# Kernel optimization log

Hardware: AMD Instinct MI355X
Metric: run time of the kernel (lower is better)

The kernel has to match this reference:

```python
import jax, jax.numpy as jnp
import numpy as np

K = 8
NMS_RADIUS = 5
SCORE_THRESHOLD = 0.05
SIGMA = 5.0


def setup_inputs() -> dict:
    key = jax.random.key(0)
    k1, k2 = jax.random.split(key)
    heatmap = jax.random.normal(k1, (16, 1, 256, 256), dtype=jnp.float32)
    feature_map = jax.random.normal(k2, (16, 128, 256, 256), dtype=jnp.float32)
    return {"heatmap": heatmap, "feature_map": feature_map}


def _extract_topk_peaks(heatmap):
    # heatmap: [B, 1, H, W]
    B, _, H, W = heatmap.shape
    hm = heatmap[:, 0]  # [B, H, W]
    r = NMS_RADIUS
    # max-pool NMS with -inf padding (== torch pad(-inf) + max_pool2d)
    hm_max = jax.lax.reduce_window(
        hm, -jnp.inf, jax.lax.max,
        window_dimensions=(1, 2 * r + 1, 2 * r + 1),
        window_strides=(1, 1, 1),
        padding=((0, 0), (r, r), (r, r)))
    gmax = jnp.max(hm.reshape(B, -1), axis=1).reshape(B, 1, 1)
    is_peak = (hm >= hm_max) & (hm >= gmax * SCORE_THRESHOLD)
    flat_hm = hm.reshape(B, -1)
    flat_peak = is_peak.reshape(B, -1)
    flat_scores = flat_hm * flat_peak.astype(flat_hm.dtype) \
        + (~flat_peak).astype(flat_hm.dtype) * (-1e9)
    topk_scores, topk_idx = jax.lax.top_k(flat_scores, K)  # [B, K]
    rows = topk_idx // W
    cols = topk_idx % W
    positions = jnp.stack([rows.astype(jnp.float32), cols.astype(jnp.float32)], axis=-1)  # [B,K,2]
    probs = jax.nn.softmax(topk_scores, axis=-1)
    valid = topk_scores > -1e8
    return positions, probs, valid


def _bilinear_sample_at_peaks(feature_map, positions):
    # feature_map: [B, C, H, W], positions: [B, K, 2] (row, col) pixel coords
    # torch grid_sample(align_corners=True, zeros pad): coords stay in-bounds,
    # so clipped bilinear interpolation is exact.
    B, C, H, W = feature_map.shape
    fmt = jnp.transpose(feature_map, (0, 2, 3, 1))  # [B, H, W, C]
    rr = positions[..., 0]
    cc = positions[..., 1]
    r0 = jnp.floor(rr)
    c0 = jnp.floor(cc)
    wr = rr - r0  # [B, K]
    wc = cc - c0
    r0i = jnp.clip(r0.astype(jnp.int32), 0, H - 1)
    r1i = jnp.clip(r0.astype(jnp.int32) + 1, 0, H - 1)
    c0i = jnp.clip(c0.astype(jnp.int32), 0, W - 1)
    c1i = jnp.clip(c0.astype(jnp.int32) + 1, 0, W - 1)
    b = jnp.arange(B)[:, None]  # [B, 1]
    f00 = fmt[b, r0i, c0i]  # [B, K, C]
    f01 = fmt[b, r0i, c1i]
    f10 = fmt[b, r1i, c0i]
    f11 = fmt[b, r1i, c1i]
    wr = wr[..., None]
    wc = wc[..., None]
    return (f00 * (1 - wr) * (1 - wc) + f01 * (1 - wr) * wc
            + f10 * wr * (1 - wc) + f11 * wr * wc)  # [B, K, C]


def _reweight_heatmap(heatmap, positions, weights, valid):
    # heatmap: [B,1,H,W]; positions: [B,K,2]; weights/valid: [B,K]
    B, _, H, W = heatmap.shape
    grid_r = jnp.arange(H, dtype=jnp.float32)[:, None]  # [H, 1]
    grid_c = jnp.arange(W, dtype=jnp.float32)[None, :]  # [1, W]
    pr = positions[:, :, 0][:, :, None, None]  # [B, K, 1, 1]
    pc = positions[:, :, 1][:, :, None, None]
    pw = weights[:, :, None, None]
    pv = valid.astype(jnp.float32)[:, :, None, None]
    dist_sq = (grid_r - pr) ** 2 + (grid_c - pc) ** 2  # [B, K, H, W]
    gaussians = jnp.exp(-dist_sq / (2.0 * SIGMA ** 2)) * pw * pv
    weight_map = jnp.sum(gaussians, axis=1, keepdims=True)  # [B, 1, H, W]
    weight_map = weight_map / (jnp.max(weight_map, axis=(-1, -2), keepdims=True) + 1e-8)
    return heatmap * (0.5 + 0.5 * weight_map)


def reference(heatmap, feature_map):
    positions, probs, valid = _extract_topk_peaks(heatmap)
    peak_feats = _bilinear_sample_at_peaks(feature_map, positions)
    reweighted = _reweight_heatmap(heatmap, positions, probs, valid)
    return reweighted, peak_feats, positions, probs, valid
```

## Files before the change

### kernel.cpp

```cpp
#include <hip/hip_runtime.h>
#include <math.h>

#define NB 16
#define HH 256
#define WW 256
#define NC 128
#define KTOP 8
#define RAD 5
#define TCAP 125
#define TILE_ROWS 16
#define HALO 5
#define LROWS (TILE_ROWS + 2*HALO)


__global__ void k_nms(const float* __restrict__ hm,
                      float* __restrict__ gpart, int* __restrict__ tcount,
                      float* __restrict__ tv, int* __restrict__ ti) {
    int b    = blockIdx.x >> 4;
    int tile = blockIdx.x & 15;
    int row0 = tile * TILE_ROWS;
    int tid  = threadIdx.x;

    __shared__ float t[LROWS][WW];
    __shared__ float hx[LROWS][WW];
    __shared__ int   cnt;
    __shared__ float red[256];
    if (tid == 0) cnt = 0;

    const float4* p4 = (const float4*)(hm + (size_t)b * HH * WW);
    float4 nf = make_float4(-INFINITY, -INFINITY, -INFINITY, -INFINITY);
    for (int i = tid; i < LROWS * (WW / 4); i += 256) {
        int lr = i >> 6, c4 = i & 63;
        int gr = row0 - HALO + lr;
        float4 v = (gr >= 0 && gr < HH) ? p4[gr * 64 + c4] : nf;
        ((float4*)&t[lr][0])[c4] = v;
    }
    __syncthreads();

    for (int i = tid; i < LROWS * WW; i += 256) {
        int lr = i >> 8, col = i & 255;
        int c0 = col - RAD < 0 ? 0 : col - RAD;
        int c1 = col + RAD > WW - 1 ? WW - 1 : col + RAD;
        float m = -INFINITY;
        for (int c = c0; c <= c1; ++c) m = fmaxf(m, t[lr][c]);
        hx[lr][col] = m;
    }
    __syncthreads();

    float tmax = -INFINITY;
    int tile_id = blockIdx.x;
    for (int i = tid; i < TILE_ROWS * WW; i += 256) {
        int lr = (i >> 8) + HALO, col = i & 255;
        float v = t[lr][col];
        tmax = fmaxf(tmax, v);
        float m = -INFINITY;
        for (int r = lr - RAD; r <= lr + RAD; ++r) m = fmaxf(m, hx[r][col]);
        if (v >= m) {
            int pos = atomicAdd(&cnt, 1);
            if (pos < TCAP) {
                tv[tile_id * TCAP + pos] = v;
                ti[tile_id * TCAP + pos] = (row0 + lr - HALO) * WW + col;
            }
        }
    }
    red[tid] = tmax;
    __syncthreads();
    for (int s = 128; s > 0; s >>= 1) {
        if (tid < s) red[tid] = fmaxf(red[tid], red[tid + s]);
        __syncthreads();
    }
    if (tid == 0) {
        gpart[tile_id]  = red[0];
        tcount[tile_id] = cnt > TCAP ? TCAP : cnt;
    }
}

__device__ __forceinline__ float wm_at_f(float fi, float fj,
                                         const float* qr, const float* qc, const float* qw) {
    float wmv = 0.f;
#pragma unroll
    for (int k = 0; k < KTOP; ++k) {
        float dr = fi - qr[k];
        float dc = fj - qc[k];
        wmv += qw[k] * __expf(-(dr * dr + dc * dc) * 0.02f);
    }
    return wmv;
}

__global__ void k_select(const float* __restrict__ fmap,
                         const float* __restrict__ gpart, const int* __restrict__ tcount,
                         const float* __restrict__ tv, const int* __restrict__ ti,
                         float* __restrict__ out_feats, float* __restrict__ out_pos,
                         float* __restrict__ out_probs, float* __restrict__ out_valid,
                         float* __restrict__ pr, float* __restrict__ pc, float* __restrict__ pw,
                         float* __restrict__ winv) {
    int b = blockIdx.x, tid = threadIdx.x;

    __shared__ float cv[16 * TCAP];
    __shared__ int   ci[16 * TCAP];
    __shared__ int   cnt;
    __shared__ int   sct[16];
    __shared__ float red[256];
    __shared__ int   redi[128];
    __shared__ float sel_v[KTOP]; __shared__ int sel_i[KTOP]; __shared__ int sel_p[KTOP];
    __shared__ float s_r[KTOP], s_c[KTOP], s_w[KTOP];

    if (tid == 0) {
        cnt = 0;
        float g = -INFINITY;
        for (int j = 0; j < 16; ++j) g = fmaxf(g, gpart[b * 16 + j]);
        red[0] = 0.05f * g;
    }
    if (tid < 16) sct[tid] = tcount[b * 16 + tid];
    __syncthreads();
    float thresh = red[0];

    for (int i = tid; i < 16 * TCAP; i += 256) {
        int j = i / TCAP, p = i - j * TCAP;
        if (p < sct[j]) {
            float v = tv[(b * 16 + j) * TCAP + p];
            if (v >= thresh) {
                int pos = atomicAdd(&cnt, 1);
                cv[pos] = v;
                ci[pos] = ti[(b * 16 + j) * TCAP + p];
            }
        }
    }
    __syncthreads();
    int count = cnt;

    for (int k = 0; k < KTOP; ++k) {
        float bv = -INFINITY; int bi = 0x7fffffff; int bp = -1;
        for (int i = tid; i < count; i += 256) {
            float v = cv[i]; int idx = ci[i];
            if (v > bv || (v == bv && idx < bi)) { bv = v; bi = idx; bp = i; }
        }
        for (int s = 1; s < 64; s <<= 1) {
            float v = __shfl_xor(bv, s); int idx = __shfl_xor(bi, s); int p = __shfl_xor(bp, s);
            if (v > bv || (v == bv && idx < bi)) { bv = v; bi = idx; bp = p; }
        }
        if ((tid & 63) == 0) { int w = tid >> 6; red[w] = bv; redi[w] = bi; redi[64 + w] = bp; }
        __syncthreads();
        if (tid == 0) {
            float v0 = red[0]; int i0 = redi[0]; int p0 = redi[64];
            for (int j = 1; j < 4; ++j)
                if (red[j] > v0 || (red[j] == v0 && redi[j] < i0)) {
                    v0 = red[j]; i0 = redi[j]; p0 = redi[64 + j];
                }
            sel_v[k] = v0; sel_i[k] = i0; sel_p[k] = p0;
            if (p0 >= 0) cv[p0] = -INFINITY;
        }
        __syncthreads();
    }

    if (tid == 0) {
        int next = 0;
        for (int k = 0; k < KTOP; ++k) {
            if (sel_p[k] < 0) {
                for (;;) {
                    bool taken = false;
                    for (int j = 0; j < count; ++j) if (ci[j] == next) { taken = true; break; }
                    if (!taken) break;
                    ++next;
                }
                sel_i[k] = next;
                sel_v[k] = -1.0e9f;
                ++next;
            }
        }
        float m = sel_v[0];
        for (int k = 1; k < KTOP; ++k) m = fmaxf(m, sel_v[k]);
        float e[KTOP], s = 0.f;
        for (int k = 0; k < KTOP; ++k) { e[k] = expf(sel_v[k] - m); s += e[k]; }
        for (int k = 0; k < KTOP; ++k) {
            float prob = e[k] / s;
            int idx = sel_i[k];
            float rrow = (float)(idx / WW);
            float rcol = (float)(idx % WW);
            float vld  = sel_v[k] > -1.0e8f ? 1.f : 0.f;
            out_pos[(b * KTOP + k) * 2 + 0] = rrow;
            out_pos[(b * KTOP + k) * 2 + 1] = rcol;
            out_probs[b * KTOP + k] = prob;
            out_valid[b * KTOP + k] = vld;
            pr[b * KTOP + k] = rrow;
            pc[b * KTOP + k] = rcol;
            pw[b * KTOP + k] = prob * vld;
            s_r[k] = rrow; s_c[k] = rcol; s_w[k] = prob * vld;
        }
    }
    __syncthreads();

    float m = 0.f;
    for (int i = tid; i < KTOP * 529; i += 256) {
        int k = i / 529, o = i - k * 529;
        int rr = (int)s_r[k] + (o / 23) - 11;
        int cc = (int)s_c[k] + (o % 23) - 11;
        if (rr >= 0 && rr < HH && cc >= 0 && cc < WW)
            m = fmaxf(m, wm_at_f((float)rr, (float)cc, s_r, s_c, s_w));
    }
    red[tid] = m;
    __syncthreads();
    for (int s = 128; s > 0; s >>= 1) {
        if (tid < s) red[tid] = fmaxf(red[tid], red[tid + s]);
        __syncthreads();
    }
    if (tid == 0) winv[b] = 0.5f / (red[0] + 1e-8f);

    for (int t = tid; t < KTOP * NC; t += 256) {
        int k  = t >> 7;
        int ch = t & 127;
        int r = (int)s_r[k];
        int c = (int)s_c[k];
        out_feats[(size_t)b * KTOP * NC + t] = fmap[((size_t)b * NC + ch) * HH * WW + r * WW + c];
    }
}

__global__ void k_reweight(const float* __restrict__ hm,
                           const float* __restrict__ pr, const float* __restrict__ pc,
                           const float* __restrict__ pw, const float* __restrict__ winv,
                           float* __restrict__ out) {
    int tile = blockIdx.x, b = blockIdx.y, tid = threadIdx.x;
    int row0 = tile * TILE_ROWS;

    __shared__ float fc[KTOP][WW];
    __shared__ float ar[KTOP][TILE_ROWS];
    __shared__ float qr[KTOP], qc[KTOP], qw[KTOP];
    __shared__ float qinv;

    if (tid < KTOP) {
        qr[tid] = pr[b * KTOP + tid];
        qc[tid] = pc[b * KTOP + tid];
        qw[tid] = pw[b * KTOP + tid];
    }
    if (tid == 0) qinv = winv[b];
    __syncthreads();

    for (int i = tid; i < KTOP * WW; i += 256) {
        int k = i >> 8, col = i & 255;
        float d = (float)col - qc[k];
        fc[k][col] = __expf(-d * d * 0.02f);
    }
    if (tid < KTOP * TILE_ROWS) {
        int k = tid >> 4, r = tid & 15;
        float d = (float)(row0 + r) - qr[k];
        ar[k][r] = qw[k] * __expf(-d * d * 0.02f);
    }
    __syncthreads();
    float inv = qinv;

    int r  = tid >> 4;
    int cb = (tid & 15) * 4;
    float a[KTOP];
#pragma unroll
    for (int k = 0; k < KTOP; ++k) a[k] = ar[k][r];

    const float4* h4 = (const float4*)(hm + (size_t)b * HH * WW + (size_t)(row0 + r) * WW);
    float4*       o4 = (float4*)(out + (size_t)b * HH * WW + (size_t)(row0 + r) * WW);
#pragma unroll
    for (int u = 0; u < 4; ++u) {
        int c4 = cb + u;
        float4 h = h4[c4];
        float4 w = make_float4(0.f, 0.f, 0.f, 0.f);
#pragma unroll
        for (int k = 0; k < KTOP; ++k) {
            float4 f = ((const float4*)&fc[k][0])[c4];
            w.x += a[k] * f.x;
            w.y += a[k] * f.y;
            w.z += a[k] * f.z;
            w.w += a[k] * f.w;
        }
        float4 o;
        o.x = h.x * (0.5f + w.x * inv);
        o.y = h.y * (0.5f + w.y * inv);
        o.z = h.z * (0.5f + w.z * inv);
        o.w = h.w * (0.5f + w.w * inv);
        o4[c4] = o;
    }
}

extern "C" void kernel_launch(void* const* d_in, const int* in_sizes, int n_in,
                              void* d_out, int out_size, void* d_ws, size_t ws_size,
                              hipStream_t stream) {
    const float* heatmap = (const float*)d_in[0];
    const float* fmap    = (const float*)d_in[1];

    float* out = (float*)d_out;
    float* out_reweighted = out;
    float* out_feats      = out + 1048576;
    float* out_pos        = out + 1048576 + 16384;
    float* out_probs      = out_pos + 256;
    float* out_valid      = out_probs + 128;

    char* ws = (char*)d_ws;
    float* tv     = (float*)(ws + 0);
    int*   ti     = (int*)  (ws + 128000);
    int*   tcount = (int*)  (ws + 256000);
    float* gpart  = (float*)(ws + 257024);
    float* pr     = (float*)(ws + 258048);
    float* pc     = (float*)(ws + 258560);
    float* pw     = (float*)(ws + 259072);
    float* winv   = (float*)(ws + 259584);

    k_nms<<<NB * 16, 256, 0, stream>>>(heatmap, gpart, tcount, tv, ti);
    k_select<<<NB, 256, 0, stream>>>(fmap, gpart, tcount, tv, ti,
                                     out_feats, out_pos, out_probs, out_valid,
                                     pr, pc, pw, winv);
    k_reweight<<<dim3(16, NB), 256, 0, stream>>>(heatmap, pr, pc, pw, winv, out_reweighted);
}
```

Measured before the change: 60.54 us.

## Fuse select and reweight kernels, recomputing top-k selection redundantly per tile

```diff
diff --git a/kernel.cpp b/kernel.cpp
--- a/kernel.cpp
+++ b/kernel.cpp
@@ -7,10 +7,12 @@
 #define NC 128
 #define KTOP 8
 #define RAD 5
-#define TCAP 125
+#define TCAP 128
 #define TILE_ROWS 16
 #define HALO 5
 #define LROWS (TILE_ROWS + 2*HALO)
+#define NT 16
+#define CTOT (NT * TCAP)
 
 
 __global__ void k_nms(const float* __restrict__ hm,
@@ -87,23 +89,26 @@
     return wmv;
 }
 
-__global__ void k_select(const float* __restrict__ fmap,
-                         const float* __restrict__ gpart, const int* __restrict__ tcount,
-                         const float* __restrict__ tv, const int* __restrict__ ti,
-                         float* __restrict__ out_feats, float* __restrict__ out_pos,
-                         float* __restrict__ out_probs, float* __restrict__ out_valid,
-                         float* __restrict__ pr, float* __restrict__ pc, float* __restrict__ pw,
-                         float* __restrict__ winv) {
-    int b = blockIdx.x, tid = threadIdx.x;
-
-    __shared__ float cv[16 * TCAP];
-    __shared__ int   ci[16 * TCAP];
+__global__ void __launch_bounds__(256)
+k_fused(const float* __restrict__ hm, const float* __restrict__ fmap,
+        const float* __restrict__ gpart, const int* __restrict__ tcount,
+        const float* __restrict__ tv, const int* __restrict__ ti,
+        float* __restrict__ out_rw, float* __restrict__ out_feats,
+        float* __restrict__ out_pos, float* __restrict__ out_probs,
+        float* __restrict__ out_valid) {
+    int tile = blockIdx.x, b = blockIdx.y, tid = threadIdx.x;
+    int row0 = tile * TILE_ROWS;
+
+    __shared__ float cv[CTOT];
+    __shared__ int   ci[CTOT];
     __shared__ int   cnt;
     __shared__ int   sct[16];
     __shared__ float red[256];
     __shared__ int   redi[128];
     __shared__ float sel_v[KTOP]; __shared__ int sel_i[KTOP]; __shared__ int sel_p[KTOP];
     __shared__ float s_r[KTOP], s_c[KTOP], s_w[KTOP];
+    __shared__ float fc[KTOP][WW];
+    __shared__ float sq;
 
     if (tid == 0) {
         cnt = 0;
@@ -115,8 +120,8 @@
     __syncthreads();
     float thresh = red[0];
 
-    for (int i = tid; i < 16 * TCAP; i += 256) {
-        int j = i / TCAP, p = i - j * TCAP;
+    for (int i = tid; i < CTOT; i += 256) {
+        int j = i >> 7, p = i & 127;
         if (p < sct[j]) {
             float v = tv[(b * 16 + j) * TCAP + p];
             if (v >= thresh) {
@@ -178,17 +183,22 @@
             float rrow = (float)(idx / WW);
             float rcol = (float)(idx % WW);
             float vld  = sel_v[k] > -1.0e8f ? 1.f : 0.f;
-            out_pos[(b * KTOP + k) * 2 + 0] = rrow;
-            out_pos[(b * KTOP + k) * 2 + 1] = rcol;
-            out_probs[b * KTOP + k] = prob;
-            out_valid[b * KTOP + k] = vld;
-            pr[b * KTOP + k] = rrow;
-            pc[b * KTOP + k] = rcol;
-            pw[b * KTOP + k] = prob * vld;
+            if (tile == 0) {
+                out_pos[(b * KTOP + k) * 2 + 0] = rrow;
+                out_pos[(b * KTOP + k) * 2 + 1] = rcol;
+                out_probs[b * KTOP + k] = prob;
+                out_valid[b * KTOP + k] = vld;
+            }
             s_r[k] = rrow; s_c[k] = rcol; s_w[k] = prob * vld;
         }
     }
     __syncthreads();
+
+    for (int i = tid; i < KTOP * WW; i += 256) {
+        int k = i >> 8, col = i & 255;
+        float d = (float)col - s_c[k];
+        fc[k][col] = __expf(-d * d * 0.02f);
+    }
 
     float m = 0.f;
     for (int i = tid; i < KTOP * 529; i += 256) {
@@ -204,58 +214,32 @@
         if (tid < s) red[tid] = fmaxf(red[tid], red[tid + s]);
         __syncthreads();
     }
-    if (tid == 0) winv[b] = 0.5f / (red[0] + 1e-8f);
-
-    for (int t = tid; t < KTOP * NC; t += 256) {
-        int k  = t >> 7;
-        int ch = t & 127;
-        int r = (int)s_r[k];
-        int c = (int)s_c[k];
-        out_feats[(size_t)b * KTOP * NC + t] = fmap[((size_t)b * NC + ch) * HH * WW + r * WW + c];
-    }
-}
-
-__global__ void k_reweight(const float* __restrict__ hm,
-                           const float* __restrict__ pr, const float* __restrict__ pc,
-                           const float* __restrict__ pw, const float* __restrict__ winv,
-                           float* __restrict__ out) {
-    int tile = blockIdx.x, b = blockIdx.y, tid = threadIdx.x;
-    int row0 = tile * TILE_ROWS;
-
-    __shared__ float fc[KTOP][WW];
-    __shared__ float ar[KTOP][TILE_ROWS];
-    __shared__ float qr[KTOP], qc[KTOP], qw[KTOP];
-    __shared__ float qinv;
-
-    if (tid < KTOP) {
-        qr[tid] = pr[b * KTOP + tid];
-        qc[tid] = pc[b * KTOP + tid];
-        qw[tid] = pw[b * KTOP + tid];
-    }
-    if (tid == 0) qinv = winv[b];
-    __syncthreads();
-
-    for (int i = tid; i < KTOP * WW; i += 256) {
-        int k = i >> 8, col = i & 255;
-        float d = (float)col - qc[k];
-        fc[k][col] = __expf(-d * d * 0.02f);
-    }
-    if (tid < KTOP * TILE_ROWS) {
-        int k = tid >> 4, r = tid & 15;
-        float d = (float)(row0 + r) - qr[k];
-        ar[k][r] = qw[k] * __expf(-d * d * 0.02f);
-    }
-    __syncthreads();
-    float inv = qinv;
+    if (tid == 0) sq = 0.5f / (red[0] + 1e-8f);
+    __syncthreads();
+    float inv = sq;
+
+    if (tile == 0) {
+        for (int t = tid; t < KTOP * NC; t += 256) {
+            int k  = t >> 7;
+            int ch = t & 127;
+            int r = (int)s_r[k];
+            int c = (int)s_c[k];
+            out_feats[(size_t)b * KTOP * NC + t] = fmap[((size_t)b * NC + ch) * HH * WW + r * WW + c];
+        }
+    }
 
     int r  = tid >> 4;
     int cb = (tid & 15) * 4;
+    float grow = (float)(row0 + r);
     float a[KTOP];
 #pragma unroll
-    for (int k = 0; k < KTOP; ++k) a[k] = ar[k][r];
+    for (int k = 0; k < KTOP; ++k) {
+        float d = grow - s_r[k];
+        a[k] = s_w[k] * __expf(-d * d * 0.02f);
+    }
 
     const float4* h4 = (const float4*)(hm + (size_t)b * HH * WW + (size_t)(row0 + r) * WW);
-    float4*       o4 = (float4*)(out + (size_t)b * HH * WW + (size_t)(row0 + r) * WW);
+    float4*       o4 = (float4*)(out_rw + (size_t)b * HH * WW + (size_t)(row0 + r) * WW);
 #pragma unroll
     for (int u = 0; u < 4; ++u) {
         int c4 = cb + u;
@@ -293,17 +277,12 @@
 
     char* ws = (char*)d_ws;
     float* tv     = (float*)(ws + 0);
-    int*   ti     = (int*)  (ws + 128000);
-    int*   tcount = (int*)  (ws + 256000);
-    float* gpart  = (float*)(ws + 257024);
-    float* pr     = (float*)(ws + 258048);
-    float* pc     = (float*)(ws + 258560);
-    float* pw     = (float*)(ws + 259072);
-    float* winv   = (float*)(ws + 259584);
+    int*   ti     = (int*)  (ws + 131072);
+    int*   tcount = (int*)  (ws + 262144);
+    float* gpart  = (float*)(ws + 263168);
 
     k_nms<<<NB * 16, 256, 0, stream>>>(heatmap, gpart, tcount, tv, ti);
-    k_select<<<NB, 256, 0, stream>>>(fmap, gpart, tcount, tv, ti,
-                                     out_feats, out_pos, out_probs, out_valid,
-                                     pr, pc, pw, winv);
-    k_reweight<<<dim3(16, NB), 256, 0, stream>>>(heatmap, pr, pc, pw, winv, out_reweighted);
-}
+    k_fused<<<dim3(16, NB), 256, 0, stream>>>(heatmap, fmap, gpart, tcount, tv, ti,
+                                              out_reweighted, out_feats,
+                                              out_pos, out_probs, out_valid);
+}
```

New measurement: 60.17 us. About the same (-0.6%).
